# Performance work log

Measured on AMD Instinct MI355X. Metric: run time of the kernel, lower is better.

Reference implementation:

```python
import jax, jax.numpy as jnp
import numpy as np

B, S = 32, 4096
HID, MEM, ATT = 512, 512, 512


def setup_inputs() -> dict:
    key = jax.random.key(0)
    k1, k2, k3, k4, k5, k6, k7 = jax.random.split(key, 7)
    scale_h = 1.0 / np.sqrt(HID)
    scale_m = 1.0 / np.sqrt(MEM)
    scale_a = 1.0 / np.sqrt(ATT)
    return {
        "hidden": jax.random.normal(k1, (B, HID), dtype=jnp.float32),
        "memory": jax.random.normal(k2, (B, S, MEM), dtype=jnp.float32),
        "mem_pad": jnp.zeros((B, S), dtype=jnp.bool_),
        "coverage": jax.random.uniform(k3, (B, S), dtype=jnp.float32),
        # params stored as (in, out) so x @ W == torch Linear(x)
        "W_h": jax.random.uniform(k4, (HID, ATT), minval=-scale_h, maxval=scale_h, dtype=jnp.float32),
        "W_m": jax.random.uniform(k5, (MEM, ATT), minval=-scale_m, maxval=scale_m, dtype=jnp.float32),
        "W_c": jax.random.uniform(k6, (ATT,), minval=-1.0, maxval=1.0, dtype=jnp.float32),
        "v": jax.random.uniform(k7, (ATT,), minval=-scale_a, maxval=scale_a, dtype=jnp.float32),
    }


def reference(hidden, memory, mem_pad, coverage, W_h, W_m, W_c, v):
    h = hidden @ W_h                                   # (B, A)
    m = jnp.einsum('bsd,da->bsa', memory, W_m)         # (B, S, A)
    c_feat = coverage[..., None] * W_c                 # (B, S, A) ; Linear(1->A) == scalar * weight row
    score = jnp.einsum('bsa,a->bs', jnp.tanh(h[:, None, :] + m + c_feat), v)  # (B, S)
    score = jnp.where(mem_pad, -jnp.inf, score)
    attn_weights = jax.nn.softmax(score, axis=-1)      # (B, S)
    context = jnp.einsum('bs,bsd->bd', attn_weights, memory)  # (B, D)
    return context, attn_weights
```

## Files before the change

kernel.cpp:

```cpp
#include <hip/hip_runtime.h>
#include <hip/hip_bf16.h>
#include <math.h>

#define BB 32
#define SS 4096
#define DMEM 512
#define DATT 512

typedef short short8 __attribute__((ext_vector_type(8)));
typedef float floatx4 __attribute__((ext_vector_type(4)));

__device__ inline short f2bf(float x) {
    unsigned u = __float_as_uint(x);
    unsigned r = (u + 0x7fffu + ((u >> 16) & 1u)) >> 16;
    return (short)(r & 0xffffu);
}

__device__ inline float fast_tanh(float x) {
    float e = __expf(2.0f * x);
    return 1.0f - 2.0f / (e + 1.0f);
}

__device__ inline void gld_lds16(const void* g, void* l) {
    __builtin_amdgcn_global_load_lds(
        (const __attribute__((address_space(1))) unsigned int*)g,
        (__attribute__((address_space(3))) unsigned int*)l, 16, 0, 0);
}


__global__ void prep_wt_kernel(const float* __restrict__ Wm, short* __restrict__ Wt) {
    const int n0 = blockIdx.x * 32;
    const int k0 = blockIdx.y * 32;
    const int t = threadIdx.x;
    const int r = t >> 5, c = t & 31;
    __shared__ float lds[32 * 33];
#pragma unroll
    for (int j = 0; j < 4; ++j) {
        int kk = r + j * 8;
        lds[kk * 33 + c] = Wm[(size_t)(k0 + kk) * 512 + n0 + c];
    }
    __syncthreads();
#pragma unroll
    for (int j = 0; j < 4; ++j) {
        int nn = r + j * 8;
        Wt[(size_t)(n0 + nn) * 512 + k0 + c] = f2bf(lds[c * 33 + nn]);
    }
}

__global__ void prep_h_kernel(const float* __restrict__ hidden, const float* __restrict__ Wh,
                              float* __restrict__ h) {
    const int b = blockIdx.x;
    const int n = blockIdx.y * 256 + threadIdx.x;
    const int kc = blockIdx.z;
    float acc = 0.f;
#pragma unroll 8
    for (int k = kc * 128; k < kc * 128 + 128; ++k)
        acc += hidden[b * 512 + k] * Wh[(size_t)k * 512 + n];
    atomicAdd(&h[b * 512 + n], acc);
}


__global__ __launch_bounds__(256, 3)
void score_kernel(const float* __restrict__ memory,
                  const float* __restrict__ coverage,
                  const short* __restrict__ Wt,
                  const float* __restrict__ h,
                  const float* __restrict__ Wc,
                  const float* __restrict__ v,
                  float* __restrict__ scoreParts) {
    const int g = blockIdx.x;
    const int inner = g & 7;
    const int nt = (g >> 3) & 3;
    const int stb = (g >> 5) * 8 + inner;
    const int st = stb & 31;
    const int b = stb >> 5;
    const int n0 = nt * 128;
    const int s0 = st * 128;

    const int tid = threadIdx.x;
    const int lane = tid & 63;
    const int wave = tid >> 6;
    const int wm = wave & 1;
    const int wn = wave >> 1;
    const int col = lane & 15;
    const int q = lane >> 4;

    __shared__ __align__(16) short tileA[128 * 64];
    __shared__ __align__(16) short tileB[2][128 * 64];
    __shared__ float covS[128];
    __shared__ float sred[2][128];

    if (tid < 128) covS[tid] = coverage[(size_t)b * SS + s0 + tid];

    const float4* gA4 = (const float4*)(memory + ((size_t)b * SS + s0) * 512);
    const char* gB = (const char*)(Wt + (size_t)n0 * 512);

    const int ar0 = tid >> 4;
    const int ac16 = tid & 15;
    const int br0 = tid >> 3;
    const int bc0 = tid & 7;

    float4 apf[8];

    floatx4 acc[4][4];
#pragma unroll
    for (int mi = 0; mi < 4; ++mi)
#pragma unroll
        for (int ni = 0; ni < 4; ++ni)
            acc[mi][ni] = (floatx4){0.f, 0.f, 0.f, 0.f};

#pragma unroll
    for (int i = 0; i < 8; ++i) {
        int row = i * 16 + ar0;
        apf[i] = gA4[(size_t)row * 128 + ac16];
    }
    {
        char* ldsB = (char*)(&tileB[0][0]) + wave * 1024;
#pragma unroll
        for (int it = 0; it < 4; ++it) {
            int row = it * 32 + br0;
            int gch = bc0 ^ (row & 7);
            gld_lds16(gB + (size_t)row * 1024 + gch * 16, ldsB + it * 4096);
        }
    }
#pragma unroll
    for (int i = 0; i < 8; ++i) {
        int row = i * 16 + ar0;
        union { __hip_bfloat162 h2; unsigned u; } p0, p1;
        p0.h2 = __float22bfloat162_rn(make_float2(apf[i].x, apf[i].y));
        p1.h2 = __float22bfloat162_rn(make_float2(apf[i].z, apf[i].w));
        uint2 w; w.x = p0.u; w.y = p1.u;
        int swzoff = (((ac16 >> 1) ^ (row & 7)) << 4) + ((ac16 & 1) << 3);
        *(uint2*)((char*)tileA + row * 128 + swzoff) = w;
    }
    __syncthreads();

    for (int kt = 0; kt < 8; ++kt) {
        if (kt < 7) {
#pragma unroll
            for (int i = 0; i < 8; ++i) {
                int row = i * 16 + ar0;
                apf[i] = gA4[(size_t)row * 128 + (kt + 1) * 16 + ac16];
            }
            char* ldsB = (char*)(&tileB[(kt + 1) & 1][0]) + wave * 1024;
#pragma unroll
            for (int it = 0; it < 4; ++it) {
                int row = it * 32 + br0;
                int gch = bc0 ^ (row & 7);
                gld_lds16(gB + (size_t)row * 1024 + (kt + 1) * 128 + gch * 16,
                          ldsB + it * 4096);
            }
        }

        const char* bbase = (const char*)(&tileB[kt & 1][0]);
#pragma unroll
        for (int ks = 0; ks < 2; ++ks) {
            short8 af[4], bf[4];
            const int cb = ks * 4 + q;
#pragma unroll
            for (int mi = 0; mi < 4; ++mi) {
                int row = wm * 64 + mi * 16 + col;
                af[mi] = *(const short8*)((const char*)tileA + row * 128 + ((cb ^ (row & 7)) * 16));
            }
#pragma unroll
            for (int ni = 0; ni < 4; ++ni) {
                int row = wn * 64 + ni * 16 + col;
                bf[ni] = *(const short8*)(bbase + row * 128 + ((cb ^ (row & 7)) * 16));
            }
#pragma unroll
            for (int mi = 0; mi < 4; ++mi)
#pragma unroll
                for (int ni = 0; ni < 4; ++ni)
                    acc[mi][ni] = __builtin_amdgcn_mfma_f32_16x16x32_bf16(af[mi], bf[ni], acc[mi][ni], 0, 0, 0);
        }

        __syncthreads();

        if (kt < 7) {
#pragma unroll
            for (int i = 0; i < 8; ++i) {
                int row = i * 16 + ar0;
                union { __hip_bfloat162 h2; unsigned u; } p0, p1;
                p0.h2 = __float22bfloat162_rn(make_float2(apf[i].x, apf[i].y));
                p1.h2 = __float22bfloat162_rn(make_float2(apf[i].z, apf[i].w));
                uint2 w; w.x = p0.u; w.y = p1.u;
                int swzoff = (((ac16 >> 1) ^ (row & 7)) << 4) + ((ac16 & 1) << 3);
                *(uint2*)((char*)tileA + row * 128 + swzoff) = w;
            }
            __syncthreads();
        }
    }

    float hv[4], wcv[4], vv[4];
#pragma unroll
    for (int ni = 0; ni < 4; ++ni) {
        int n = n0 + wn * 64 + ni * 16 + col;
        hv[ni] = h[b * 512 + n];
        wcv[ni] = Wc[n];
        vv[ni] = v[n];
    }
    float rowAcc[4][4];
#pragma unroll
    for (int mi = 0; mi < 4; ++mi)
#pragma unroll
        for (int r = 0; r < 4; ++r)
            rowAcc[mi][r] = 0.f;
#pragma unroll
    for (int mi = 0; mi < 4; ++mi) {
#pragma unroll
        for (int r = 0; r < 4; ++r) {
            float cv = covS[wm * 64 + mi * 16 + q * 4 + r];
#pragma unroll
            for (int ni = 0; ni < 4; ++ni) {
                float val = acc[mi][ni][r] + hv[ni] + cv * wcv[ni];
                rowAcc[mi][r] += fast_tanh(val) * vv[ni];
            }
        }
    }
#pragma unroll
    for (int off = 1; off < 16; off <<= 1)
#pragma unroll
        for (int mi = 0; mi < 4; ++mi)
#pragma unroll
            for (int r = 0; r < 4; ++r)
                rowAcc[mi][r] += __shfl_xor(rowAcc[mi][r], off, 64);

    if (col == 0) {
#pragma unroll
        for (int mi = 0; mi < 4; ++mi)
#pragma unroll
            for (int r = 0; r < 4; ++r)
                sred[wn][wm * 64 + mi * 16 + q * 4 + r] = rowAcc[mi][r];
    }
    __syncthreads();
    if (tid < 128)
        scoreParts[(size_t)nt * BB * SS + (size_t)b * SS + s0 + tid] =
            sred[0][tid] + sred[1][tid];
}

__global__ void softmax_kernel(const float* __restrict__ scoreParts,
                               const unsigned char* __restrict__ pad,
                               float* __restrict__ attn_out) {
    const int b = blockIdx.x;
    const int tid = threadIdx.x;
    const int wave = tid >> 6, lane = tid & 63;
    __shared__ float redMax[16];
    __shared__ float redSum[16];

    float vals[4];
    float mx = -INFINITY;
#pragma unroll
    for (int i = 0; i < 4; ++i) {
        size_t idx = (size_t)b * SS + tid + i * 1024;
        float s = scoreParts[idx] + scoreParts[(size_t)BB * SS + idx]
                + scoreParts[2 * (size_t)BB * SS + idx] + scoreParts[3 * (size_t)BB * SS + idx];
        if (pad[idx]) s = -INFINITY;
        vals[i] = s;
        mx = fmaxf(mx, s);
    }
#pragma unroll
    for (int off = 32; off >= 1; off >>= 1) mx = fmaxf(mx, __shfl_xor(mx, off, 64));
    if (lane == 0) redMax[wave] = mx;
    __syncthreads();
    float gmax = -INFINITY;
#pragma unroll
    for (int w = 0; w < 16; ++w) gmax = fmaxf(gmax, redMax[w]);

    float sum = 0.f;
#pragma unroll
    for (int i = 0; i < 4; ++i) {
        float e = __expf(vals[i] - gmax);
        vals[i] = e;
        sum += e;
    }
#pragma unroll
    for (int off = 32; off >= 1; off >>= 1) sum += __shfl_xor(sum, off, 64);
    if (lane == 0) redSum[wave] = sum;
    __syncthreads();
    float gsum = 0.f;
#pragma unroll
    for (int w = 0; w < 16; ++w) gsum += redSum[w];
    const float inv = 1.0f / gsum;
#pragma unroll
    for (int i = 0; i < 4; ++i)
        attn_out[(size_t)b * SS + tid + i * 1024] = vals[i] * inv;
}

__global__ __launch_bounds__(256)
void context_kernel(const float* __restrict__ memory,
                    const float* __restrict__ attn,
                    float* __restrict__ ctx) {
    const int sc = blockIdx.x;
    const int dh = blockIdx.y;
    const int b  = blockIdx.z;
    const int t = threadIdx.x;
    const int c = t & 63;
    const int r = t >> 6;

    __shared__ float wS[128];
    __shared__ float4 red[3][64];

    if (t < 128) wS[t] = attn[(size_t)b * SS + sc * 128 + t];
    __syncthreads();

    const float4* m4 = (const float4*)(memory + ((size_t)b * SS + sc * 128) * DMEM) + dh * 64 + c;
    float4 acc = {0.f, 0.f, 0.f, 0.f};
#pragma unroll 8
    for (int i = 0; i < 32; ++i) {
        int row = i * 4 + r;
        float w = wS[row];
        float4 f = m4[(size_t)row * 128];
        acc.x += w * f.x; acc.y += w * f.y; acc.z += w * f.z; acc.w += w * f.w;
    }
    if (r > 0) red[r - 1][c] = acc;
    __syncthreads();
    if (r == 0) {
#pragma unroll
        for (int j = 0; j < 3; ++j) {
            float4 o = red[j][c];
            acc.x += o.x; acc.y += o.y; acc.z += o.z; acc.w += o.w;
        }
        float* dst = &ctx[b * 512 + dh * 256 + c * 4];
        atomicAdd(dst + 0, acc.x);
        atomicAdd(dst + 1, acc.y);
        atomicAdd(dst + 2, acc.z);
        atomicAdd(dst + 3, acc.w);
    }
}

extern "C" void kernel_launch(void* const* d_in, const int* in_sizes, int n_in,
                              void* d_out, int out_size, void* d_ws, size_t ws_size,
                              hipStream_t stream) {
    (void)in_sizes; (void)n_in; (void)out_size; (void)ws_size;
    const float* hidden   = (const float*)d_in[0];
    const float* memory   = (const float*)d_in[1];
    const unsigned char* mem_pad = (const unsigned char*)d_in[2];
    const float* coverage = (const float*)d_in[3];
    const float* Wh       = (const float*)d_in[4];
    const float* Wm       = (const float*)d_in[5];
    const float* Wc       = (const float*)d_in[6];
    const float* v        = (const float*)d_in[7];

    char* ws = (char*)d_ws;
    short* Wt    = (short*)ws;
    float* h     = (float*)(ws + 512 * 1024);
    float* parts = (float*)(ws + 576 * 1024);

    float* ctx  = (float*)d_out;
    float* attn = (float*)d_out + BB * 512;

    hipMemsetAsync(ctx, 0, BB * 512 * sizeof(float), stream);
    hipMemsetAsync(h, 0, BB * 512 * sizeof(float), stream);
    prep_wt_kernel<<<dim3(16, 16), dim3(256), 0, stream>>>(Wm, Wt);
    prep_h_kernel<<<dim3(32, 2, 4), dim3(256), 0, stream>>>(hidden, Wh, h);
    score_kernel<<<dim3(4096), dim3(256), 0, stream>>>(memory, coverage, Wt, h, Wc, v, parts);
    softmax_kernel<<<dim3(BB), dim3(1024), 0, stream>>>(parts, mem_pad, attn);
    context_kernel<<<dim3(32, 2, BB), dim3(256), 0, stream>>>(memory, attn, ctx);
}
```

Before: 499.9 us.

## Fuse score, split-softmax and context into one kernel with full-N tiles

The score GEMM, softmax and context reduction are merged into one kernel. Each block computes all 512 attention columns for a 128-row sequence tile, so the memory tile is read and converted once instead of four times. The block then computes a local max and sum (flash-style), writes unnormalized probabilities and a partial context vector, and a small combine kernel rescales these to produce the final context and attention weights. This removes the repeated memory reads for the four N tiles and the separate pass over memory for context. In exchange it uses 512-thread blocks with about 148KB of LDS and 128 accumulator registers per thread, which lowers occupancy. The context pass may hit L2 because it rereads the same memory tile.

```diff
diff --git a/kernel.cpp b/kernel.cpp
--- a/kernel.cpp
+++ b/kernel.cpp
@@ -60,21 +60,23 @@
 }
 
 
-__global__ __launch_bounds__(256, 3)
-void score_kernel(const float* __restrict__ memory,
+#define FK_MISC (147456)
+
+__global__ __launch_bounds__(512, 2)
+void fused_kernel(const float* __restrict__ memory,
                   const float* __restrict__ coverage,
+                  const unsigned char* __restrict__ pad,
                   const short* __restrict__ Wt,
                   const float* __restrict__ h,
                   const float* __restrict__ Wc,
                   const float* __restrict__ v,
-                  float* __restrict__ scoreParts) {
-    const int g = blockIdx.x;
-    const int inner = g & 7;
-    const int nt = (g >> 3) & 3;
-    const int stb = (g >> 5) * 8 + inner;
-    const int st = stb & 31;
-    const int b = stb >> 5;
-    const int n0 = nt * 128;
+                  float* __restrict__ pOut,
+                  float* __restrict__ mWS,
+                  float* __restrict__ lWS,
+                  float* __restrict__ ctxPart) {
+    const int blk = blockIdx.x;
+    const int b = blk >> 5;
+    const int st = blk & 31;
     const int s0 = st * 128;
 
     const int tid = threadIdx.x;
@@ -85,50 +87,51 @@
     const int col = lane & 15;
     const int q = lane >> 4;
 
-    __shared__ __align__(16) short tileA[128 * 64];
-    __shared__ __align__(16) short tileB[2][128 * 64];
-    __shared__ float covS[128];
-    __shared__ float sred[2][128];
+    __shared__ __align__(16) char smem[FK_MISC + 4096];
+    short* tileB0 = (short*)smem;
+    short* tileB1 = (short*)(smem + 65536);
+    short* tileA  = (short*)(smem + 131072);
+    float* covS   = (float*)(smem + FK_MISC);
+    float* sred   = (float*)(smem + FK_MISC + 512);
+    float* scoreS = (float*)(smem + FK_MISC + 2560);
+    float* pS     = (float*)(smem + FK_MISC + 3072);
+    float* mlS    = (float*)(smem + FK_MISC + 3584);
+    float4* red4  = (float4*)smem;
 
     if (tid < 128) covS[tid] = coverage[(size_t)b * SS + s0 + tid];
 
     const float4* gA4 = (const float4*)(memory + ((size_t)b * SS + s0) * 512);
-    const char* gB = (const char*)(Wt + (size_t)n0 * 512);
+    const char* gB = (const char*)Wt;
 
     const int ar0 = tid >> 4;
     const int ac16 = tid & 15;
-    const int br0 = tid >> 3;
-    const int bc0 = tid & 7;
-
-    float4 apf[8];
-
-    floatx4 acc[4][4];
+
+    float4 apf[4];
+
+    floatx4 acc[4][8];
 #pragma unroll
     for (int mi = 0; mi < 4; ++mi)
 #pragma unroll
-        for (int ni = 0; ni < 4; ++ni)
+        for (int ni = 0; ni < 8; ++ni)
             acc[mi][ni] = (floatx4){0.f, 0.f, 0.f, 0.f};
 
 #pragma unroll
-    for (int i = 0; i < 8; ++i) {
-        int row = i * 16 + ar0;
-        apf[i] = gA4[(size_t)row * 128 + ac16];
-    }
-    {
-        char* ldsB = (char*)(&tileB[0][0]) + wave * 1024;
-#pragma unroll
-        for (int it = 0; it < 4; ++it) {
-            int row = it * 32 + br0;
-            int gch = bc0 ^ (row & 7);
-            gld_lds16(gB + (size_t)row * 1024 + gch * 16, ldsB + it * 4096);
-        }
-    }
-#pragma unroll
-    for (int i = 0; i < 8; ++i) {
-        int row = i * 16 + ar0;
+    for (int p = 0; p < 4; ++p)
+        apf[p] = gA4[(size_t)(p * 32 + ar0) * 128 + ac16];
+#pragma unroll
+    for (int it = 0; it < 8; ++it) {
+        int ci = (it * 8 + wave) * 64 + lane;
+        int row = ci >> 3;
+        int gch = (ci & 7) ^ (row & 7);
+        gld_lds16(gB + (size_t)row * 1024 + gch * 16,
+                  (char*)tileB0 + (it * 8 + wave) * 1024);
+    }
+#pragma unroll
+    for (int p = 0; p < 4; ++p) {
+        int row = p * 32 + ar0;
         union { __hip_bfloat162 h2; unsigned u; } p0, p1;
-        p0.h2 = __float22bfloat162_rn(make_float2(apf[i].x, apf[i].y));
-        p1.h2 = __float22bfloat162_rn(make_float2(apf[i].z, apf[i].w));
+        p0.h2 = __float22bfloat162_rn(make_float2(apf[p].x, apf[p].y));
+        p1.h2 = __float22bfloat162_rn(make_float2(apf[p].z, apf[p].w));
         uint2 w; w.x = p0.u; w.y = p1.u;
         int swzoff = (((ac16 >> 1) ^ (row & 7)) << 4) + ((ac16 & 1) << 3);
         *(uint2*)((char*)tileA + row * 128 + swzoff) = w;
@@ -138,24 +141,23 @@
     for (int kt = 0; kt < 8; ++kt) {
         if (kt < 7) {
 #pragma unroll
-            for (int i = 0; i < 8; ++i) {
-                int row = i * 16 + ar0;
-                apf[i] = gA4[(size_t)row * 128 + (kt + 1) * 16 + ac16];
-            }
-            char* ldsB = (char*)(&tileB[(kt + 1) & 1][0]) + wave * 1024;
-#pragma unroll
-            for (int it = 0; it < 4; ++it) {
-                int row = it * 32 + br0;
-                int gch = bc0 ^ (row & 7);
+            for (int p = 0; p < 4; ++p)
+                apf[p] = gA4[(size_t)(p * 32 + ar0) * 128 + (kt + 1) * 16 + ac16];
+            char* ldsB = (char*)(((kt + 1) & 1) ? tileB1 : tileB0);
+#pragma unroll
+            for (int it = 0; it < 8; ++it) {
+                int ci = (it * 8 + wave) * 64 + lane;
+                int row = ci >> 3;
+                int gch = (ci & 7) ^ (row & 7);
                 gld_lds16(gB + (size_t)row * 1024 + (kt + 1) * 128 + gch * 16,
-                          ldsB + it * 4096);
-            }
-        }
-
-        const char* bbase = (const char*)(&tileB[kt & 1][0]);
+                          ldsB + (it * 8 + wave) * 1024);
+            }
+        }
+
+        const char* bbase = (const char*)((kt & 1) ? tileB1 : tileB0);
 #pragma unroll
         for (int ks = 0; ks < 2; ++ks) {
-            short8 af[4], bf[4];
+            short8 af[4], bf[8];
             const int cb = ks * 4 + q;
 #pragma unroll
             for (int mi = 0; mi < 4; ++mi) {
@@ -163,14 +165,14 @@
                 af[mi] = *(const short8*)((const char*)tileA + row * 128 + ((cb ^ (row & 7)) * 16));
             }
 #pragma unroll
-            for (int ni = 0; ni < 4; ++ni) {
-                int row = wn * 64 + ni * 16 + col;
+            for (int ni = 0; ni < 8; ++ni) {
+                int row = wn * 128 + ni * 16 + col;
                 bf[ni] = *(const short8*)(bbase + row * 128 + ((cb ^ (row & 7)) * 16));
             }
 #pragma unroll
             for (int mi = 0; mi < 4; ++mi)
 #pragma unroll
-                for (int ni = 0; ni < 4; ++ni)
+                for (int ni = 0; ni < 8; ++ni)
                     acc[mi][ni] = __builtin_amdgcn_mfma_f32_16x16x32_bf16(af[mi], bf[ni], acc[mi][ni], 0, 0, 0);
         }
 
@@ -178,11 +180,11 @@
 
         if (kt < 7) {
 #pragma unroll
-            for (int i = 0; i < 8; ++i) {
-                int row = i * 16 + ar0;
+            for (int p = 0; p < 4; ++p) {
+                int row = p * 32 + ar0;
                 union { __hip_bfloat162 h2; unsigned u; } p0, p1;
-                p0.h2 = __float22bfloat162_rn(make_float2(apf[i].x, apf[i].y));
-                p1.h2 = __float22bfloat162_rn(make_float2(apf[i].z, apf[i].w));
+                p0.h2 = __float22bfloat162_rn(make_float2(apf[p].x, apf[p].y));
+                p1.h2 = __float22bfloat162_rn(make_float2(apf[p].z, apf[p].w));
                 uint2 w; w.x = p0.u; w.y = p1.u;
                 int swzoff = (((ac16 >> 1) ^ (row & 7)) << 4) + ((ac16 & 1) << 3);
                 *(uint2*)((char*)tileA + row * 128 + swzoff) = w;
@@ -191,10 +193,10 @@
         }
     }
 
-    float hv[4], wcv[4], vv[4];
-#pragma unroll
-    for (int ni = 0; ni < 4; ++ni) {
-        int n = n0 + wn * 64 + ni * 16 + col;
+    float hv[8], wcv[8], vv[8];
+#pragma unroll
+    for (int ni = 0; ni < 8; ++ni) {
+        int n = wn * 128 + ni * 16 + col;
         hv[ni] = h[b * 512 + n];
         wcv[ni] = Wc[n];
         vv[ni] = v[n];
@@ -211,7 +213,7 @@
         for (int r = 0; r < 4; ++r) {
             float cv = covS[wm * 64 + mi * 16 + q * 4 + r];
 #pragma unroll
-            for (int ni = 0; ni < 4; ++ni) {
+            for (int ni = 0; ni < 8; ++ni) {
                 float val = acc[mi][ni][r] + hv[ni] + cv * wcv[ni];
                 rowAcc[mi][r] += fast_tanh(val) * vv[ni];
             }
@@ -230,101 +232,107 @@
         for (int mi = 0; mi < 4; ++mi)
 #pragma unroll
             for (int r = 0; r < 4; ++r)
-                sred[wn][wm * 64 + mi * 16 + q * 4 + r] = rowAcc[mi][r];
-    }
-    __syncthreads();
-    if (tid < 128)
-        scoreParts[(size_t)nt * BB * SS + (size_t)b * SS + s0 + tid] =
-            sred[0][tid] + sred[1][tid];
-}
-
-__global__ void softmax_kernel(const float* __restrict__ scoreParts,
-                               const unsigned char* __restrict__ pad,
-                               float* __restrict__ attn_out) {
+                sred[wn * 128 + wm * 64 + mi * 16 + q * 4 + r] = rowAcc[mi][r];
+    }
+    __syncthreads();
+
+    if (tid < 128) {
+        float sc = sred[tid] + sred[128 + tid] + sred[256 + tid] + sred[384 + tid];
+        if (pad[(size_t)b * SS + s0 + tid]) sc = -INFINITY;
+        scoreS[tid] = sc;
+    }
+    __syncthreads();
+    if (tid < 64) {
+        float mx = fmaxf(scoreS[tid], scoreS[tid + 64]);
+#pragma unroll
+        for (int off = 32; off >= 1; off >>= 1) mx = fmaxf(mx, __shfl_xor(mx, off, 64));
+        if (tid == 0) mlS[0] = mx;
+    }
+    __syncthreads();
+    const float mtile = mlS[0];
+    if (tid < 128) pS[tid] = __expf(scoreS[tid] - mtile);
+    __syncthreads();
+    if (tid < 64) {
+        float sm = pS[tid] + pS[tid + 64];
+#pragma unroll
+        for (int off = 32; off >= 1; off >>= 1) sm += __shfl_xor(sm, off, 64);
+        if (tid == 0) mlS[1] = sm;
+    }
+    __syncthreads();
+
+    if (tid < 128) pOut[(size_t)b * SS + s0 + tid] = pS[tid];
+    if (tid == 0) {
+        mWS[b * 32 + st] = mtile;
+        lWS[b * 32 + st] = mlS[1];
+    }
+
+    const int sg = tid >> 7;
+    const int dc = tid & 127;
+    const float4* m4 = (const float4*)(memory + ((size_t)b * SS + s0) * 512);
+    float4 a4 = {0.f, 0.f, 0.f, 0.f};
+#pragma unroll 8
+    for (int i = 0; i < 32; ++i) {
+        int s = sg * 32 + i;
+        float w = pS[s];
+        float4 f = m4[(size_t)s * 128 + dc];
+        a4.x += w * f.x; a4.y += w * f.y; a4.z += w * f.z; a4.w += w * f.w;
+    }
+    red4[sg * 128 + dc] = a4;
+    __syncthreads();
+    if (tid < 128) {
+        float4 r0 = red4[tid], r1 = red4[128 + tid], r2 = red4[256 + tid], r3 = red4[384 + tid];
+        float4 o;
+        o.x = r0.x + r1.x + r2.x + r3.x;
+        o.y = r0.y + r1.y + r2.y + r3.y;
+        o.z = r0.z + r1.z + r2.z + r3.z;
+        o.w = r0.w + r1.w + r2.w + r3.w;
+        ((float4*)(ctxPart + ((size_t)(b * 32 + st)) * 512))[tid] = o;
+    }
+}
+
+__global__ __launch_bounds__(512)
+void combine_kernel(const float* __restrict__ mWS,
+                    const float* __restrict__ lWS,
+                    const float* __restrict__ ctxPart,
+                    float* __restrict__ ctx,
+                    float* __restrict__ attn) {
     const int b = blockIdx.x;
     const int tid = threadIdx.x;
-    const int wave = tid >> 6, lane = tid & 63;
-    __shared__ float redMax[16];
-    __shared__ float redSum[16];
-
-    float vals[4];
-    float mx = -INFINITY;
-#pragma unroll
-    for (int i = 0; i < 4; ++i) {
-        size_t idx = (size_t)b * SS + tid + i * 1024;
-        float s = scoreParts[idx] + scoreParts[(size_t)BB * SS + idx]
-                + scoreParts[2 * (size_t)BB * SS + idx] + scoreParts[3 * (size_t)BB * SS + idx];
-        if (pad[idx]) s = -INFINITY;
-        vals[i] = s;
-        mx = fmaxf(mx, s);
-    }
-#pragma unroll
-    for (int off = 32; off >= 1; off >>= 1) mx = fmaxf(mx, __shfl_xor(mx, off, 64));
-    if (lane == 0) redMax[wave] = mx;
-    __syncthreads();
-    float gmax = -INFINITY;
-#pragma unroll
-    for (int w = 0; w < 16; ++w) gmax = fmaxf(gmax, redMax[w]);
-
-    float sum = 0.f;
-#pragma unroll
-    for (int i = 0; i < 4; ++i) {
-        float e = __expf(vals[i] - gmax);
-        vals[i] = e;
-        sum += e;
-    }
-#pragma unroll
-    for (int off = 32; off >= 1; off >>= 1) sum += __shfl_xor(sum, off, 64);
-    if (lane == 0) redSum[wave] = sum;
-    __syncthreads();
-    float gsum = 0.f;
-#pragma unroll
-    for (int w = 0; w < 16; ++w) gsum += redSum[w];
-    const float inv = 1.0f / gsum;
-#pragma unroll
-    for (int i = 0; i < 4; ++i)
-        attn_out[(size_t)b * SS + tid + i * 1024] = vals[i] * inv;
-}
-
-__global__ __launch_bounds__(256)
-void context_kernel(const float* __restrict__ memory,
-                    const float* __restrict__ attn,
-                    float* __restrict__ ctx) {
-    const int sc = blockIdx.x;
-    const int dh = blockIdx.y;
-    const int b  = blockIdx.z;
-    const int t = threadIdx.x;
-    const int c = t & 63;
-    const int r = t >> 6;
-
-    __shared__ float wS[128];
-    __shared__ float4 red[3][64];
-
-    if (t < 128) wS[t] = attn[(size_t)b * SS + sc * 128 + t];
-    __syncthreads();
-
-    const float4* m4 = (const float4*)(memory + ((size_t)b * SS + sc * 128) * DMEM) + dh * 64 + c;
-    float4 acc = {0.f, 0.f, 0.f, 0.f};
+    __shared__ float scaleS[32];
+    __shared__ float gS[2];
+
+    if (tid < 64) {
+        float mv = (tid < 32) ? mWS[b * 32 + tid] : -INFINITY;
+#pragma unroll
+        for (int off = 32; off >= 1; off >>= 1) mv = fmaxf(mv, __shfl_xor(mv, off, 64));
+        if (tid == 0) gS[0] = mv;
+    }
+    __syncthreads();
+    const float gmax = gS[0];
+    if (tid < 64) {
+        float sc = 0.f, lv = 0.f;
+        if (tid < 32) {
+            sc = __expf(mWS[b * 32 + tid] - gmax);
+            scaleS[tid] = sc;
+            lv = lWS[b * 32 + tid] * sc;
+        }
+#pragma unroll
+        for (int off = 32; off >= 1; off >>= 1) lv += __shfl_xor(lv, off, 64);
+        if (tid == 0) gS[1] = lv;
+    }
+    __syncthreads();
+    const float inv = 1.0f / gS[1];
+
+    float facc = 0.f;
 #pragma unroll 8
-    for (int i = 0; i < 32; ++i) {
-        int row = i * 4 + r;
-        float w = wS[row];
-        float4 f = m4[(size_t)row * 128];
-        acc.x += w * f.x; acc.y += w * f.y; acc.z += w * f.z; acc.w += w * f.w;
-    }
-    if (r > 0) red[r - 1][c] = acc;
-    __syncthreads();
-    if (r == 0) {
-#pragma unroll
-        for (int j = 0; j < 3; ++j) {
-            float4 o = red[j][c];
-            acc.x += o.x; acc.y += o.y; acc.z += o.z; acc.w += o.w;
-        }
-        float* dst = &ctx[b * 512 + dh * 256 + c * 4];
-        atomicAdd(dst + 0, acc.x);
-        atomicAdd(dst + 1, acc.y);
-        atomicAdd(dst + 2, acc.z);
-        atomicAdd(dst + 3, acc.w);
+    for (int st = 0; st < 32; ++st)
+        facc += ctxPart[((size_t)(b * 32 + st)) * 512 + tid] * scaleS[st];
+    ctx[b * 512 + tid] = facc * inv;
+
+#pragma unroll
+    for (int j = 0; j < 8; ++j) {
+        size_t idx = (size_t)b * SS + j * 512 + tid;
+        attn[idx] = attn[idx] * scaleS[(j * 512 + tid) >> 7] * inv;
     }
 }
 
@@ -342,18 +350,19 @@
     const float* v        = (const float*)d_in[7];
 
     char* ws = (char*)d_ws;
-    short* Wt    = (short*)ws;
-    float* h     = (float*)(ws + 512 * 1024);
-    float* parts = (float*)(ws + 576 * 1024);
+    short* Wt      = (short*)ws;
+    float* h       = (float*)(ws + 512 * 1024);
+    float* mWS     = (float*)(ws + 576 * 1024);
+    float* lWS     = (float*)(ws + 580 * 1024);
+    float* ctxPart = (float*)(ws + 584 * 1024);
 
     float* ctx  = (float*)d_out;
     float* attn = (float*)d_out + BB * 512;
 
-    hipMemsetAsync(ctx, 0, BB * 512 * sizeof(float), stream);
     hipMemsetAsync(h, 0, BB * 512 * sizeof(float), stream);
     prep_wt_kernel<<<dim3(16, 16), dim3(256), 0, stream>>>(Wm, Wt);
     prep_h_kernel<<<dim3(32, 2, 4), dim3(256), 0, stream>>>(hidden, Wh, h);
-    score_kernel<<<dim3(4096), dim3(256), 0, stream>>>(memory, coverage, Wt, h, Wc, v, parts);
-    softmax_kernel<<<dim3(BB), dim3(1024), 0, stream>>>(parts, mem_pad, attn);
-    context_kernel<<<dim3(32, 2, BB), dim3(256), 0, stream>>>(memory, attn, ctx);
-}
+    fused_kernel<<<dim3(BB * 32), dim3(512), 0, stream>>>(
+        memory, coverage, mem_pad, Wt, h, Wc, v, attn, mWS, lWS, ctxPart);
+    combine_kernel<<<dim3(BB), dim3(512), 0, stream>>>(mWS, lWS, ctxPart, ctx, attn);
+}
```

Result: faster. 472.0 us (-5.6%).
